# Optimization experiments

Measured on AMD Instinct MI355X. Metric: run time of the kernel, lower is better.

Reference implementation:

```python
import jax, jax.numpy as jnp
import numpy as np
import math

B, L, IN, HID, NLAYERS, AA = 16, 512, 512, 512, 6, 21
KAPPA_ADD = 5.0


def _sru_layer(x, W, v, b):
    # x: [L, B, din]; W: [din, 2*HID*k]; v, b: [2(gate f/r), 2(dir), HID]
    Lx, Bx, din = x.shape
    d = HID
    k = W.shape[1] // (2 * d)  # 4 if projecting residual, 3 if residual = input
    U = (x @ W).reshape(Lx, Bx, 2, d, k)
    res = U[..., 3] if k == 4 else x.reshape(Lx, Bx, 2, d)
    # time-flip direction 1 so a single scan handles both directions
    flip = lambda a: jnp.concatenate([a[:, :, :1], a[::-1, :, 1:]], axis=2)
    u0, u1, u2, resf = flip(U[..., 0]), flip(U[..., 1]), flip(U[..., 2]), flip(res)
    vf, vr = v[0], v[1]
    bf, br = b[0], b[1]

    def step(c, t):
        u0t, u1t, u2t, rt = t
        f = jax.nn.sigmoid(u1t + vf * c + bf)
        c1 = f * c + (1.0 - f) * u0t
        r = jax.nn.sigmoid(u2t + vr * c1 + br)
        h = r * c1 + (1.0 - r) * rt
        return c1, h

    c0 = jnp.zeros((Bx, 2, d), x.dtype)
    _, H = jax.lax.scan(step, c0, (u0, u1, u2, resf))
    return flip(H).reshape(Lx, Bx, 2 * d)


def setup_inputs():
    key = jax.random.key(0)
    inp = {}
    inp['input'] = jax.random.normal(jax.random.fold_in(key, 0), (B, L, IN), jnp.float32)
    inp['hidden'] = jnp.zeros((NLAYERS, B, 2 * HID), jnp.float32)
    for l in range(NLAYERS):
        din = IN if l == 0 else 2 * HID
        k = 4 if din != 2 * HID else 3
        inp[f'sru_w{l}'] = jax.random.normal(jax.random.fold_in(key, 10 + l), (din, 2 * HID * k), jnp.float32) * (1.0 / math.sqrt(din))
        inp[f'sru_v{l}'] = jax.random.normal(jax.random.fold_in(key, 20 + l), (2, 2, HID), jnp.float32) * 0.1
        inp[f'sru_b{l}'] = jnp.zeros((2, 2, HID), jnp.float32)

    def lin(seed, din, dout):
        w = jax.random.normal(jax.random.fold_in(key, seed), (din, dout), jnp.float32) * (1.0 / math.sqrt(din))
        return w, jnp.zeros((dout,), jnp.float32)

    inp['fc1_logits_w'], inp['fc1_logits_b'] = lin(30, 2 * HID, HID)
    inp['fc2_logits_w'], inp['fc2_logits_b'] = lin(31, HID, AA)
    inp['fc1_angles_w'], inp['fc1_angles_b'] = lin(32, 2 * HID, HID)
    inp['fc2_means_w'], inp['fc2_means_b'] = lin(33, HID, 2)
    inp['fc2_kappas_w'], inp['fc2_kappas_b'] = lin(34, HID, 2)
    return inp


def reference(input, hidden, sru_w0, sru_v0, sru_b0, sru_w1, sru_v1, sru_b1, sru_w2, sru_v2, sru_b2, sru_w3, sru_v3, sru_b3, sru_w4, sru_v4, sru_b4, sru_w5, sru_v5, sru_b5, fc1_logits_w, fc1_logits_b, fc2_logits_w, fc2_logits_b, fc1_angles_w, fc1_angles_b, fc2_means_w, fc2_means_b, fc2_kappas_w, fc2_kappas_b):
    x = input.transpose(1, 0, 2)  # [L, B, IN]
    ws = [sru_w0, sru_w1, sru_w2, sru_w3, sru_w4, sru_w5]
    vs = [sru_v0, sru_v1, sru_v2, sru_v3, sru_v4, sru_v5]
    bs = [sru_b0, sru_b1, sru_b2, sru_b3, sru_b4, sru_b5]
    for W, v, b in zip(ws, vs, bs):
        x = _sru_layer(x, W, v, b)
    sru_out = x.transpose(1, 0, 2)  # [B, L, 2*HID]
    h_log = sru_out @ fc1_logits_w + fc1_logits_b
    output_logits = jax.nn.log_softmax(h_log @ fc2_logits_w + fc2_logits_b, axis=-1)
    h_ang = sru_out @ fc1_angles_w + fc1_angles_b
    output_means = jnp.tanh(h_ang @ fc2_means_w + fc2_means_b) * math.pi
    output_kappas = KAPPA_ADD + jax.nn.softplus(h_ang @ fc2_kappas_w + fc2_kappas_b)
    return (output_logits, output_means, output_kappas)
```

## Files before the change

kernel.cpp:

```cpp
#include <hip/hip_runtime.h>

typedef __attribute__((ext_vector_type(8))) short short8;
typedef __attribute__((ext_vector_type(4))) float f32x4;

__device__ __forceinline__ ushort f2bf(float x) {
  unsigned u = __builtin_bit_cast(unsigned, x);
  u = (u + 0x7fffu + ((u >> 16) & 1u)) >> 16;
  return (ushort)u;
}
__device__ __forceinline__ float bf2f(ushort x) {
  return __builtin_bit_cast(float, ((unsigned)x) << 16);
}

#define AS1CP(p) ((const __attribute__((address_space(1))) unsigned int*)(p))
#define AS3CP(p) ((__attribute__((address_space(3))) unsigned int*)(p))
#define GLDS(g, l, SZ) __builtin_amdgcn_global_load_lds(AS1CP(g), AS3CP(l), SZ, 0, 0)

__global__ __launch_bounds__(256) void k_cvt(const float* __restrict__ in,
                                             ushort* __restrict__ out, int n4) {
  int i = blockIdx.x * 256 + threadIdx.x;
  if (i >= n4) return;
  float4 v = reinterpret_cast<const float4*>(in)[i];
  ushort4 o;
  o.x = f2bf(v.x); o.y = f2bf(v.y); o.z = f2bf(v.z); o.w = f2bf(v.w);
  reinterpret_cast<ushort4*>(out)[i] = o;
}

__global__ __launch_bounds__(256) void k_transpose(const float* __restrict__ W,
                                                   ushort* __restrict__ Wt,
                                                   int N, int K) {
  __shared__ float tile[32][33];
  int bx = blockIdx.x * 32;
  int by = blockIdx.y * 32;
  int tx = threadIdx.x, ty = threadIdx.y;
#pragma unroll
  for (int i = 0; i < 32; i += 8)
    tile[ty + i][tx] = W[(size_t)(by + ty + i) * N + bx + tx];
  __syncthreads();
#pragma unroll
  for (int i = 0; i < 32; i += 8)
    Wt[(size_t)(bx + ty + i) * K + by + tx] = f2bf(tile[tx][ty + i]);
}

template <int KKp>
__global__ __launch_bounds__(256) void k_transpose_sru(const float* __restrict__ W,
                                                       ushort* __restrict__ Wt,
                                                       int N, int K) {
  __shared__ float tile[32][33];
  int bx = blockIdx.x * 32;
  int by = blockIdx.y * 32;
  int tx = threadIdx.x, ty = threadIdx.y;
#pragma unroll
  for (int i = 0; i < 32; i += 8)
    tile[ty + i][tx] = W[(size_t)(by + ty + i) * N + bx + tx];
  __syncthreads();
#pragma unroll
  for (int i = 0; i < 32; i += 8) {
    int c = bx + ty + i;
    int ch = c / KKp, j = c - ch * KKp;
    int nc = j * 1024 + ch;
    Wt[(size_t)nc * K + by + tx] = f2bf(tile[tx][ty + i]);
  }
}

template <int BF16OUT>
__global__ __launch_bounds__(256) void k_gemm(const ushort* __restrict__ A,
                                              const ushort* __restrict__ Bt,
                                              void* __restrict__ Cv,
                                              int K, int N) {
  __shared__ __align__(16) ushort lsA[2][2][4096];
  __shared__ __align__(16) ushort lsB[2][2][4096];
  const int tid = threadIdx.x;
  const int bm = blockIdx.x, bn = blockIdx.y;
  const int w = tid >> 6, l = tid & 63;
  const int wm = (w >> 1) * 64, wn = (w & 1) * 64;
  const int lr = l & 15, lg = l >> 4;
  f32x4 acc[4][4] = {};
  const int srow = tid >> 2;
  const int scol = (((tid & 3) ^ ((srow >> 1) & 3))) * 8;
  const ushort* Ag = A + (size_t)(bm * 128 + srow) * K + scol;
  const ushort* Bg = Bt + (size_t)(bn * 128 + srow) * K + scol;
  const int nt = K >> 6;
  const int rxor = (lr >> 1) & 3;

#define GEMM_ISSUE(SL, KT)                                                  \
  {                                                                         \
    GLDS(Ag + (KT), &lsA[SL][0][w * 512], 16);                              \
    GLDS(Ag + (size_t)64 * K + (KT), &lsA[SL][0][2048 + w * 512], 16);      \
    GLDS(Bg + (KT), &lsB[SL][0][w * 512], 16);                              \
    GLDS(Bg + (size_t)64 * K + (KT), &lsB[SL][0][2048 + w * 512], 16);      \
    GLDS(Ag + (KT) + 32, &lsA[SL][1][w * 512], 16);                         \
    GLDS(Ag + (size_t)64 * K + (KT) + 32, &lsA[SL][1][2048 + w * 512], 16); \
    GLDS(Bg + (KT) + 32, &lsB[SL][1][w * 512], 16);                         \
    GLDS(Bg + (size_t)64 * K + (KT) + 32, &lsB[SL][1][2048 + w * 512], 16); \
  }

  GEMM_ISSUE(0, 0);
  for (int t = 0; t < nt; ++t) {
    const int cur = t & 1;
    if (t + 1 < nt) {
      GEMM_ISSUE(cur ^ 1, (t + 1) * 64);
      asm volatile("s_waitcnt vmcnt(8)" ::: "memory");
    } else {
      asm volatile("s_waitcnt vmcnt(0)" ::: "memory");
    }
    asm volatile("s_barrier" ::: "memory");
#pragma unroll
    for (int kk = 0; kk < 2; ++kk) {
      short8 af[4], bfr[4];
#pragma unroll
      for (int i = 0; i < 4; ++i)
        af[i] = *(const short8*)&lsA[cur][kk][(wm + i * 16 + lr) * 32 + ((lg ^ rxor) * 8)];
#pragma unroll
      for (int j = 0; j < 4; ++j)
        bfr[j] = *(const short8*)&lsB[cur][kk][(wn + j * 16 + lr) * 32 + ((lg ^ rxor) * 8)];
#pragma unroll
      for (int i = 0; i < 4; ++i)
#pragma unroll
        for (int j = 0; j < 4; ++j)
          acc[i][j] = __builtin_amdgcn_mfma_f32_16x16x32_bf16(af[i], bfr[j], acc[i][j], 0, 0, 0);
    }
    asm volatile("s_barrier" ::: "memory");
  }
#undef GEMM_ISSUE
  const size_t cbase = (size_t)(bm * 128 + wm + lg * 4) * N + bn * 128 + wn + lr;
  if (BF16OUT) {
    ushort* Cb = (ushort*)Cv + cbase;
#pragma unroll
    for (int i = 0; i < 4; ++i)
#pragma unroll
      for (int j = 0; j < 4; ++j)
#pragma unroll
        for (int r = 0; r < 4; ++r)
          Cb[(size_t)(i * 16 + r) * N + j * 16] = f2bf(acc[i][j][r]);
  } else {
    float* Cb = (float*)Cv + cbase;
#pragma unroll
    for (int i = 0; i < 4; ++i)
#pragma unroll
      for (int j = 0; j < 4; ++j)
#pragma unroll
        for (int r = 0; r < 4; ++r)
          Cb[(size_t)(i * 16 + r) * N + j * 16] = acc[i][j][r];
  }
}

template <int WRITE_NEXT>
__global__ __launch_bounds__(64, 1) void sru_rec10(const ushort* __restrict__ U,
                                                   const ushort* __restrict__ Rp,
                                                   const float* __restrict__ v,
                                                   const float* __restrict__ bb,
                                                   ushort* __restrict__ H,
                                                   ushort* __restrict__ Hres) {
  const size_t PL = (size_t)1024 * 8192;
  const int lane = threadIdx.x;
  const int blk = blockIdx.x;
  const int b = blk >> 4, cg = blk & 15;
  const int ch = cg * 64 + lane;
  const int dir = ch >> 9;
  const float vf = v[ch], vr = v[1024 + ch];
  const float bfv = bb[ch], brv = bb[1024 + ch];
  const float vfn = -vf, vrn = -vr;
  const float kf0 = -bfv, kr0 = -brv;
  const size_t rowoff = (size_t)ch * 8192 + b * 512;
  const ushort* U0 = U + rowoff;
  const ushort* U1 = U0 + PL;
  const ushort* U2 = U0 + 2 * PL;
  const ushort* Rb = Rp + rowoff;
  ushort* Hb = H + (size_t)b * 512 * 1024 + ch;
  ushort* Hr = Hres + rowoff;

  short8 q0[8], q1[8], q2[8], qr[8];

#define SR_ISSUE(J, TI)                                                        \
  {                                                                            \
    const int tb_ = dir ? (504 - (TI) * 8) : ((TI) * 8);                       \
    q0[J] = *(const short8*)(U0 + tb_);                                        \
    q1[J] = *(const short8*)(U1 + tb_);                                        \
    q2[J] = *(const short8*)(U2 + tb_);                                        \
    qr[J] = *(const short8*)(Rb + tb_);                                        \
  }

#define SR_COMP(J, TI)                                                         \
  {                                                                            \
    const int tb_ = dir ? (504 - (TI) * 8) : ((TI) * 8);                       \
    short8 hv = {};                                                            \
    _Pragma("unroll")                                                          \
    for (int s = 0; s < 8; ++s) {                                              \
      const int e0 = s, e1 = 7 - s;                                            \
      const int e = dir ? e1 : e0;                                             \
      float u0 = bf2f((ushort)(dir ? q0[J][e1] : q0[J][e0]));                  \
      float u1 = bf2f((ushort)(dir ? q1[J][e1] : q1[J][e0]));                  \
      float u2 = bf2f((ushort)(dir ? q2[J][e1] : q2[J][e0]));                  \
      float uR = bf2f((ushort)(dir ? qr[J][e1] : qr[J][e0]));                  \
      float ef = __expf(__builtin_fmaf(vfn, c, kf0 - u1));                     \
      float f = __builtin_amdgcn_rcpf(1.f + ef);                               \
      c = __builtin_fmaf(f, c - u0, u0);                                       \
      float er = __expf(__builtin_fmaf(vrn, c, kr0 - u2));                     \
      float r = __builtin_amdgcn_rcpf(1.f + er);                               \
      float hh = __builtin_fmaf(r, c - uR, uR);                                \
      ushort hb = f2bf(hh);                                                    \
      Hb[(size_t)(tb_ + e) * 1024] = hb;                                       \
      if (WRITE_NEXT) { if (dir) hv[e1] = (short)hb; else hv[e0] = (short)hb; }\
    }                                                                          \
    if (WRITE_NEXT) *(short8*)(Hr + tb_) = hv;                                 \
  }

#define SR_W(N) asm volatile("s_waitcnt vmcnt(" #N ")" ::: "memory");

  SR_ISSUE(0, 0) SR_ISSUE(1, 1) SR_ISSUE(2, 2) SR_ISSUE(3, 3)
  SR_ISSUE(4, 4) SR_ISSUE(5, 5) SR_ISSUE(6, 6)
  float c = 0.f;
  SR_ISSUE(7, 7)   SR_W(28) SR_COMP(0, 0)
  SR_ISSUE(0, 8)   SR_W(32) SR_COMP(1, 1)
  SR_ISSUE(1, 9)   SR_W(40) SR_COMP(2, 2)
  SR_ISSUE(2, 10)  SR_W(48) SR_COMP(3, 3)
  SR_ISSUE(3, 11)  SR_W(56) SR_COMP(4, 4)
  SR_ISSUE(4, 12)  SR_W(63) SR_COMP(5, 5)
  SR_ISSUE(5, 13)  SR_W(63) SR_COMP(6, 6)
  SR_ISSUE(6, 14)  SR_W(63) SR_COMP(7, 7)
#pragma unroll 1
  for (int ii = 1; ii < 7; ++ii) {
#define TILE_J(J)                                                              \
    {                                                                          \
      const int i = ii * 8 + (J);                                              \
      SR_ISSUE((((J) + 7) & 7), i + 7)                                         \
      SR_W(63)                                                                 \
      SR_COMP(J, i)                                                            \
    }
    TILE_J(0) TILE_J(1) TILE_J(2) TILE_J(3)
    TILE_J(4) TILE_J(5) TILE_J(6) TILE_J(7)
#undef TILE_J
  }
  SR_ISSUE(7, 63)
  SR_W(63) SR_COMP(0, 56)
  SR_W(63) SR_COMP(1, 57)
  SR_W(63) SR_COMP(2, 58)
  SR_W(63) SR_COMP(3, 59)
  SR_W(63) SR_COMP(4, 60)
  SR_W(63) SR_COMP(5, 61)
  SR_W(48) SR_COMP(6, 62)
  SR_W(48) SR_COMP(7, 63)
#undef SR_ISSUE
#undef SR_COMP
#undef SR_W
}

__global__ __launch_bounds__(256) void k_buildW2(const float* __restrict__ w2l,
                                                 const float* __restrict__ w2m,
                                                 const float* __restrict__ w2k,
                                                 ushort* __restrict__ Wt2) {
  int i = blockIdx.x * 256 + threadIdx.x;
  if (i >= 128 * 1024) return;
  int n = i >> 10, k = i & 1023;
  float vv = 0.f;
  if (n < 21 && k < 512) vv = w2l[k * 21 + n];
  else if (n >= 21 && n < 23 && k >= 512) vv = w2m[(k - 512) * 2 + (n - 21)];
  else if (n >= 23 && n < 25 && k >= 512) vv = w2k[(k - 512) * 2 + (n - 23)];
  Wt2[i] = f2bf(vv);
}

__global__ __launch_bounds__(64) void k_bias25(const float* __restrict__ b1l,
                                               const float* __restrict__ b1a,
                                               const float* __restrict__ w2l,
                                               const float* __restrict__ b2l,
                                               const float* __restrict__ w2m,
                                               const float* __restrict__ b2m,
                                               const float* __restrict__ w2k,
                                               const float* __restrict__ b2k,
                                               float* __restrict__ b2adj) {
  int o = threadIdx.x;
  if (o >= 25) return;
  float s;
  if (o < 21) {
    s = b2l[o];
    for (int k = 0; k < 512; ++k) s += b1l[k] * w2l[k * 21 + o];
  } else if (o < 23) {
    s = b2m[o - 21];
    for (int k = 0; k < 512; ++k) s += b1a[k] * w2m[k * 2 + (o - 21)];
  } else {
    s = b2k[o - 23];
    for (int k = 0; k < 512; ++k) s += b1a[k] * w2k[k * 2 + (o - 23)];
  }
  b2adj[o] = s;
}

__global__ __launch_bounds__(64) void k_act(const float* __restrict__ T,
                                            const float* __restrict__ b2adj,
                                            float* __restrict__ out) {
  const int row = blockIdx.x;
  const int lane = threadIdx.x;
  float myv = 0.f;
  if (lane < 25) myv = T[(size_t)row * 128 + lane] + b2adj[lane];
  float x = (lane < 21) ? myv : -1e30f;
#pragma unroll
  for (int off = 32; off; off >>= 1) x = fmaxf(x, __shfl_xor(x, off));
  float e = (lane < 21) ? expf(myv - x) : 0.f;
#pragma unroll
  for (int off = 32; off; off >>= 1) e += __shfl_xor(e, off);
  float lse = x + logf(e);
  if (lane < 21) {
    out[(size_t)row * 21 + lane] = myv - lse;
  } else if (lane < 23) {
    out[172032 + row * 2 + (lane - 21)] = tanhf(myv) * 3.14159265358979323846f;
  } else if (lane < 25) {
    float sp = (myv > 20.f) ? myv : log1pf(expf(myv));
    out[188416 + row * 2 + (lane - 23)] = 5.f + sp;
  }
}

extern "C" void kernel_launch(void* const* d_in, const int* in_sizes, int n_in,
                              void* d_out, int out_size, void* d_ws, size_t ws_size,
                              hipStream_t stream) {
  (void)in_sizes; (void)n_in; (void)out_size; (void)ws_size;
  const float* input = (const float*)d_in[0];
  const float* sw[6]; const float* sv[6]; const float* sb[6];
  for (int l = 0; l < 6; ++l) {
    sw[l] = (const float*)d_in[2 + 3 * l];
    sv[l] = (const float*)d_in[3 + 3 * l];
    sb[l] = (const float*)d_in[4 + 3 * l];
  }
  const float* fc1lw = (const float*)d_in[20];
  const float* fc1lb = (const float*)d_in[21];
  const float* fc2lw = (const float*)d_in[22];
  const float* fc2lb = (const float*)d_in[23];
  const float* fc1aw = (const float*)d_in[24];
  const float* fc1ab = (const float*)d_in[25];
  const float* fc2mw = (const float*)d_in[26];
  const float* fc2mb = (const float*)d_in[27];
  const float* fc2kw = (const float*)d_in[28];
  const float* fc2kb = (const float*)d_in[29];

  char* ws = (char*)d_ws;
  ushort* U = (ushort*)ws;
  ushort* Hcat2 = (ushort*)ws;
  float* T = (float*)(ws + 33554432);
  ushort* HresA = (ushort*)(ws + 67108864);
  ushort* HresB = (ushort*)(ws + 83886080);
  ushort* H0 = (ushort*)(ws + 134217728);
  ushort* H1 = (ushort*)(ws + 150994944);
  ushort* X0 = (ushort*)(ws + 167772160);
  const size_t wbase = 176160768;
  ushort* Wtl[6];
  Wtl[0] = (ushort*)(ws + wbase);
  for (int l = 1; l < 6; ++l)
    Wtl[l] = (ushort*)(ws + wbase + 4194304 + (size_t)(l - 1) * 6291456);
  ushort* Wfc = (ushort*)(ws + wbase + 4194304 + 5ull * 6291456);
  ushort* Wt2 = (ushort*)(ws + wbase + 37748736);
  float* b2adj = (float*)(ws + wbase + 38010880);

  k_cvt<<<4096, 256, 0, stream>>>(input, X0, 8192 * 512 / 4);
  k_buildW2<<<512, 256, 0, stream>>>(fc2lw, fc2mw, fc2kw, Wt2);
  k_bias25<<<1, 64, 0, stream>>>(fc1lb, fc1ab, fc2lw, fc2lb, fc2mw, fc2mb,
                                 fc2kw, fc2kb, b2adj);

  k_transpose_sru<4><<<dim3(128, 16), dim3(32, 8), 0, stream>>>(sw[0], Wtl[0], 4096, 512);
  for (int l = 1; l < 6; ++l)
    k_transpose_sru<3><<<dim3(96, 32), dim3(32, 8), 0, stream>>>(sw[l], Wtl[l], 3072, 1024);
  k_transpose<<<dim3(16, 32), dim3(32, 8), 0, stream>>>(fc1lw, Wfc, 512, 1024);
  k_transpose<<<dim3(16, 32), dim3(32, 8), 0, stream>>>(fc1aw, Wfc + (size_t)512 * 1024, 512, 1024);

  const size_t PL = (size_t)1024 * 8192;
  for (int l = 0; l < 6; ++l) {
    const ushort* Ain = (l == 0) ? X0 : ((l & 1) ? H0 : H1);
    ushort* Hout = (l & 1) ? H1 : H0;
    int K = (l == 0) ? 512 : 1024;
    int NF = (l == 0) ? 4096 : 3072;
    k_gemm<1><<<dim3(NF / 128, 64), 256, 0, stream>>>(Wtl[l], Ain, U, K, 8192);
    const ushort* Rp = (l == 0) ? (U + 3 * PL) : ((l & 1) ? HresA : HresB);
    ushort* Hro = (l & 1) ? HresB : HresA;
    if (l < 5)
      sru_rec10<1><<<256, 64, 0, stream>>>(U, Rp, sv[l], sb[l], Hout, Hro);
    else
      sru_rec10<0><<<256, 64, 0, stream>>>(U, Rp, sv[l], sb[l], Hout, Hro);
  }

  k_gemm<1><<<dim3(64, 8), 256, 0, stream>>>(H1, Wfc, Hcat2, 1024, 1024);

  k_gemm<0><<<dim3(64, 1), 256, 0, stream>>>(Hcat2, Wt2, T, 1024, 128);

  k_act<<<8192, 64, 0, stream>>>(T, b2adj, (float*)d_out);
}
```

Baseline: 750.3 us.

## Switch GEMM to triple-buffered 32-wide K stages with a single barrier per step

The GEMM main loop moves from a double buffer with two 32-wide K sub-tiles per 64-wide step to a three-slot ring of 32-wide K stages, prefetched two stages ahead. Each iteration now uses a single barrier, and the next load is issued after that barrier into the slot freed two steps earlier. The aim is more load/compute overlap and fewer barriers per unit of K, with LDS use going from four sub-tile buffers to three. In exchange, each barrier covers half as much MFMA work, and the loop runs twice as many iterations, each with its own wait.

Result: slower. 769.0 us (+2.5%).

```diff
diff --git a/kernel.cpp b/kernel.cpp
--- a/kernel.cpp
+++ b/kernel.cpp
@@ -68,8 +68,8 @@
                                               const ushort* __restrict__ Bt,
                                               void* __restrict__ Cv,
                                               int K, int N) {
-  __shared__ __align__(16) ushort lsA[2][2][4096];
-  __shared__ __align__(16) ushort lsB[2][2][4096];
+  __shared__ __align__(16) ushort lsA[3][4096];
+  __shared__ __align__(16) ushort lsB[3][4096];
   const int tid = threadIdx.x;
   const int bm = blockIdx.x, bn = blockIdx.y;
   const int w = tid >> 6, l = tid & 63;
@@ -80,47 +80,42 @@
   const int scol = (((tid & 3) ^ ((srow >> 1) & 3))) * 8;
   const ushort* Ag = A + (size_t)(bm * 128 + srow) * K + scol;
   const ushort* Bg = Bt + (size_t)(bn * 128 + srow) * K + scol;
-  const int nt = K >> 6;
+  const int nt = K >> 5;
   const int rxor = (lr >> 1) & 3;
 
-#define GEMM_ISSUE(SL, KT)                                                  \
-  {                                                                         \
-    GLDS(Ag + (KT), &lsA[SL][0][w * 512], 16);                              \
-    GLDS(Ag + (size_t)64 * K + (KT), &lsA[SL][0][2048 + w * 512], 16);      \
-    GLDS(Bg + (KT), &lsB[SL][0][w * 512], 16);                              \
-    GLDS(Bg + (size_t)64 * K + (KT), &lsB[SL][0][2048 + w * 512], 16);      \
-    GLDS(Ag + (KT) + 32, &lsA[SL][1][w * 512], 16);                         \
-    GLDS(Ag + (size_t)64 * K + (KT) + 32, &lsA[SL][1][2048 + w * 512], 16); \
-    GLDS(Bg + (KT) + 32, &lsB[SL][1][w * 512], 16);                         \
-    GLDS(Bg + (size_t)64 * K + (KT) + 32, &lsB[SL][1][2048 + w * 512], 16); \
+#define GEMM_ISSUE(SL, KT)                                           \
+  {                                                                  \
+    GLDS(Ag + (KT), &lsA[SL][w * 512], 16);                          \
+    GLDS(Ag + (size_t)64 * K + (KT), &lsA[SL][2048 + w * 512], 16);  \
+    GLDS(Bg + (KT), &lsB[SL][w * 512], 16);                          \
+    GLDS(Bg + (size_t)64 * K + (KT), &lsB[SL][2048 + w * 512], 16);  \
   }
 
   GEMM_ISSUE(0, 0);
+  GEMM_ISSUE(1, 32);
+  int sl2 = 2;
+  int cur = 0;
   for (int t = 0; t < nt; ++t) {
-    const int cur = t & 1;
-    if (t + 1 < nt) {
-      GEMM_ISSUE(cur ^ 1, (t + 1) * 64);
-      asm volatile("s_waitcnt vmcnt(8)" ::: "memory");
-    } else {
+    if (t + 1 < nt)
+      asm volatile("s_waitcnt vmcnt(4)" ::: "memory");
+    else
       asm volatile("s_waitcnt vmcnt(0)" ::: "memory");
-    }
     asm volatile("s_barrier" ::: "memory");
-#pragma unroll
-    for (int kk = 0; kk < 2; ++kk) {
-      short8 af[4], bfr[4];
-#pragma unroll
-      for (int i = 0; i < 4; ++i)
-        af[i] = *(const short8*)&lsA[cur][kk][(wm + i * 16 + lr) * 32 + ((lg ^ rxor) * 8)];
+    if (t + 2 < nt) GEMM_ISSUE(sl2, (t + 2) * 32);
+    short8 af[4], bfr[4];
+#pragma unroll
+    for (int i = 0; i < 4; ++i)
+      af[i] = *(const short8*)&lsA[cur][(wm + i * 16 + lr) * 32 + ((lg ^ rxor) * 8)];
+#pragma unroll
+    for (int j = 0; j < 4; ++j)
+      bfr[j] = *(const short8*)&lsB[cur][(wn + j * 16 + lr) * 32 + ((lg ^ rxor) * 8)];
+#pragma unroll
+    for (int i = 0; i < 4; ++i)
 #pragma unroll
       for (int j = 0; j < 4; ++j)
-        bfr[j] = *(const short8*)&lsB[cur][kk][(wn + j * 16 + lr) * 32 + ((lg ^ rxor) * 8)];
-#pragma unroll
-      for (int i = 0; i < 4; ++i)
-#pragma unroll
-        for (int j = 0; j < 4; ++j)
-          acc[i][j] = __builtin_amdgcn_mfma_f32_16x16x32_bf16(af[i], bfr[j], acc[i][j], 0, 0, 0);
-    }
-    asm volatile("s_barrier" ::: "memory");
+        acc[i][j] = __builtin_amdgcn_mfma_f32_16x16x32_bf16(af[i], bfr[j], acc[i][j], 0, 0, 0);
+    cur = (cur == 2) ? 0 : cur + 1;
+    sl2 = (sl2 == 2) ? 0 : sl2 + 1;
   }
 #undef GEMM_ISSUE
   const size_t cbase = (size_t)(bm * 128 + wm + lg * 4) * N + bn * 128 + wn + lr;
```
